# Kernel tuning notes

Hardware: AMD Instinct MI355X
Metric: run time of the kernel (lower is better)

The kernel has to match this reference:

```python
import jax, jax.numpy as jnp
import numpy as np

B, N, C, CD, R = 8, 16384, 32, 256, 32


def setup_inputs() -> dict:
    key = jax.random.key(0)
    ks = jax.random.split(key, 12)
    f32 = jnp.float32
    p = lambda k, shape, s=0.05: jax.random.normal(k, shape, f32) * s
    return {
        "features": jax.random.normal(ks[0], (B, C, N), f32),
        "coords": jax.random.normal(ks[1], (B, 3, N), f32),
        "condition": jax.random.normal(ks[2], (B, CD), f32),
        "conv1_w": p(ks[3], (C, C, 3, 3, 3)), "conv1_b": jnp.zeros((C,), f32),
        "gn1_g": jnp.ones((C,), f32), "gn1_b": jnp.zeros((C,), f32),
        "mod1_w": p(ks[4], (2 * C, CD)),
        "mod1_b": jnp.concatenate([jnp.ones((C,)), jnp.zeros((C,))]).astype(f32),
        "conv2_w": p(ks[5], (C, C, 3, 3, 3)), "conv2_b": jnp.zeros((C,), f32),
        "gn2_g": jnp.ones((C,), f32), "gn2_b": jnp.zeros((C,), f32),
        "mod2_w": p(ks[6], (2 * C, CD)),
        "mod2_b": jnp.concatenate([jnp.ones((C,)), jnp.zeros((C,))]).astype(f32),
        "se_w1": p(ks[7], (C // 8, C)), "se_w2": p(ks[8], (C, C // 8)),
        "pc_w": p(ks[9], (C, C)), "pc_b": jnp.zeros((C,), f32),
        "gnp_g": jnp.ones((C,), f32), "gnp_b": jnp.zeros((C,), f32),
        "modp_w": p(ks[10], (2 * C, CD)),
        "modp_b": jnp.concatenate([jnp.ones((C,)), jnp.zeros((C,))]).astype(f32),
    }


def group_norm(x, g, b, G=8, eps=1e-5):
    shape = x.shape
    xg = x.reshape(shape[0], G, -1)
    m = xg.mean(-1, keepdims=True)
    v = xg.var(-1, keepdims=True)
    xn = ((xg - m) * jax.lax.rsqrt(v + eps)).reshape(shape)
    bshape = (1, shape[1]) + (1,) * (x.ndim - 2)
    return xn * g.reshape(bshape) + b.reshape(bshape)


def adagn(x, c, g, b, mw, mb):
    # GroupNorm then scale/shift from SiLU(c) @ Linear
    x = group_norm(x, g, b)
    m = jax.nn.silu(c) @ mw.T + mb  # (B, 2C)
    scale, shift = jnp.split(m, 2, axis=1)
    bshape = (x.shape[0], x.shape[1]) + (1,) * (x.ndim - 2)
    return x * scale.reshape(bshape) + shift.reshape(bshape)


def voxelize(features, coords, r):
    # scatter-average point features into r^3 grid; coords detached as in torch
    coords = jax.lax.stop_gradient(coords)
    nc = coords - coords.mean(2, keepdims=True)
    denom = jnp.max(jnp.linalg.norm(nc, axis=1, keepdims=True), axis=2, keepdims=True) * 2.0
    nc = nc / denom + 0.5
    nc = jnp.clip(nc * r, 0, r - 1)  # (B,3,N) continuous in [0, r-1]
    vc = jnp.round(nc).astype(jnp.int32)
    idx = (vc[:, 0] * r + vc[:, 1]) * r + vc[:, 2]  # (B,N) flat voxel ids

    def per_batch(f, i):
        s = jax.ops.segment_sum(f.T, i, num_segments=r ** 3)  # (V, D)
        cnt = jax.ops.segment_sum(jnp.ones(i.shape, f.dtype), i, num_segments=r ** 3)
        return (s / jnp.maximum(cnt, 1.0)[:, None]).T.reshape(f.shape[0], r, r, r)

    vox = jax.vmap(per_batch)(features, idx)  # (B, D, r, r, r)
    return vox, nc


def devoxelize(vox, coords, r):
    # trilinear gather of voxel features back to points
    Bv, D = vox.shape[:2]
    flat = vox.reshape(Bv, D, r * r * r)
    lo = jnp.floor(coords)
    frac = coords - lo
    lo = lo.astype(jnp.int32)
    hi = jnp.minimum(lo + 1, r - 1)
    gather = jax.vmap(lambda f, i: f[:, i])  # per-batch (D,V)[:, (N,)] -> (D,N)
    out = jnp.zeros((Bv, D, coords.shape[2]), vox.dtype)
    for dx in (0, 1):
        ix = hi[:, 0] if dx else lo[:, 0]
        wx = frac[:, 0] if dx else 1.0 - frac[:, 0]
        for dy in (0, 1):
            iy = hi[:, 1] if dy else lo[:, 1]
            wy = frac[:, 1] if dy else 1.0 - frac[:, 1]
            for dz in (0, 1):
                iz = hi[:, 2] if dz else lo[:, 2]
                wz = frac[:, 2] if dz else 1.0 - frac[:, 2]
                idx = (ix * r + iy) * r + iz
                out = out + gather(flat, idx) * (wx * wy * wz)[:, None, :]
    return out


def conv3d(x, w, b):
    y = jax.lax.conv_general_dilated(x, w, (1, 1, 1), 'SAME',
                                     dimension_numbers=('NCDHW', 'OIDHW', 'NCDHW'))
    return y + b[None, :, None, None, None]


def reference(features, coords, condition, conv1_w, conv1_b, gn1_g, gn1_b, mod1_w,
              mod1_b, conv2_w, conv2_b, gn2_g, gn2_b, mod2_w, mod2_b, se_w1, se_w2,
              pc_w, pc_b, gnp_g, gnp_b, modp_w, modp_b):
    vox, nc = voxelize(features, coords, R)
    v = conv3d(vox, conv1_w, conv1_b)
    v = jax.nn.silu(adagn(v, condition, gn1_g, gn1_b, mod1_w, mod1_b))
    v = conv3d(v, conv2_w, conv2_b)
    v = adagn(v, condition, gn2_g, gn2_b, mod2_w, mod2_b)
    # SE3d squeeze-excite
    s = jax.nn.sigmoid(jax.nn.relu(v.mean((2, 3, 4)) @ se_w1.T) @ se_w2.T)
    v = v * s[:, :, None, None, None]
    vfeat = devoxelize(v, nc, R)  # (B, C, N)
    # point branch: 1x1 conv + AdaGN + SiLU
    px = jnp.einsum('bdn,od->bon', features, pc_w) + pc_b[None, :, None]
    px = jax.nn.silu(adagn(px, condition, gnp_g, gnp_b, modp_w, modp_b))
    return vfeat + px
```

## Files before the change

kernel.cpp:

```cpp
#include <hip/hip_runtime.h>
#include <math.h>

#define DEV_INLINE __device__ __forceinline__

namespace {

typedef unsigned short u16;
typedef unsigned int u32;
typedef __attribute__((ext_vector_type(8))) short short8v;
typedef __attribute__((ext_vector_type(4))) float f32x4;
typedef __attribute__((ext_vector_type(16))) float f32x16;

constexpr int Bn = 8, Cn = 32, Nn = 16384, Rn = 32, Vn = Rn * Rn * Rn;

DEV_INLINE float siluf(float x) { return x / (1.0f + __expf(-x)); }
DEV_INLINE float bf2f(u16 u) { union { u32 i; float f; } x; x.i = (u32)u << 16; return x.f; }
DEV_INLINE u16 f2bf(float f) {
  union { float f; u32 i; } x; x.f = f;
  return (u16)((x.i + 0x7FFFu + ((x.i >> 16) & 1u)) >> 16);
}
DEV_INLINE u32 pack2(float a, float b) { return (u32)f2bf(a) | ((u32)f2bf(b) << 16); }
DEV_INLINE void unpack8(uint4 u, float* f) {
  f[0] = bf2f(u.x & 0xffff); f[1] = bf2f(u.x >> 16);
  f[2] = bf2f(u.y & 0xffff); f[3] = bf2f(u.y >> 16);
  f[4] = bf2f(u.z & 0xffff); f[5] = bf2f(u.z >> 16);
  f[6] = bf2f(u.w & 0xffff); f[7] = bf2f(u.w >> 16);
}

__global__ void k_cpart1(const float* __restrict__ coords, float* __restrict__ csum) {
  int blk = blockIdx.x;
  int b = blk >> 3, s = blk & 7;
  int t = threadIdx.x;
  const float* cb = coords + (size_t)b * 3 * Nn;
  int n0 = s * 2048;
  float sx = 0.f, sy = 0.f, sz = 0.f;
  for (int n = n0 + t; n < n0 + 2048; n += 256) {
    sx += cb[n]; sy += cb[Nn + n]; sz += cb[2 * Nn + n];
  }
  #pragma unroll
  for (int m = 1; m <= 32; m <<= 1) {
    sx += __shfl_xor(sx, m); sy += __shfl_xor(sy, m); sz += __shfl_xor(sz, m);
  }
  __shared__ float rs[3][4];
  if ((t & 63) == 0) { rs[0][t >> 6] = sx; rs[1][t >> 6] = sy; rs[2][t >> 6] = sz; }
  __syncthreads();
  if (t < 3) atomicAdd(&csum[b * 4 + t], rs[t][0] + rs[t][1] + rs[t][2] + rs[t][3]);
}

__global__ void k_cpart2(const float* __restrict__ coords, const float* __restrict__ csum,
                         int* __restrict__ cmax) {
  int blk = blockIdx.x;
  int b = blk >> 3, s = blk & 7;
  int t = threadIdx.x;
  const float* cb = coords + (size_t)b * 3 * Nn;
  const float invn = 1.0f / (float)Nn;
  float mx = csum[b * 4] * invn, my = csum[b * 4 + 1] * invn, mz = csum[b * 4 + 2] * invn;
  int n0 = s * 2048;
  float mq = 0.f;
  for (int n = n0 + t; n < n0 + 2048; n += 256) {
    float x = cb[n] - mx, y = cb[Nn + n] - my, z = cb[2 * Nn + n] - mz;
    mq = fmaxf(mq, x * x + y * y + z * z);
  }
  #pragma unroll
  for (int m = 1; m <= 32; m <<= 1) mq = fmaxf(mq, __shfl_xor(mq, m));
  __shared__ float rm[4];
  if ((t & 63) == 0) rm[t >> 6] = mq;
  __syncthreads();
  if (t == 0) {
    float v = fmaxf(fmaxf(rm[0], rm[1]), fmaxf(rm[2], rm[3]));
    atomicMax(cmax + b, __float_as_int(v));
  }
}

__global__ void k_cfinal(const float* __restrict__ coords, const float* __restrict__ csum,
                         const int* __restrict__ cmax, float* __restrict__ nc,
                         int* __restrict__ vidx, int* __restrict__ hist) {
  int i = blockIdx.x * 256 + threadIdx.x;
  int b = i >> 14, n = i & (Nn - 1);
  const float* cb = coords + (size_t)b * 3 * Nn;
  const float invn = 1.0f / (float)Nn;
  float mx = csum[b * 4] * invn, my = csum[b * 4 + 1] * invn, mz = csum[b * 4 + 2] * invn;
  float inv = 1.0f / (2.0f * sqrtf(__int_as_float(cmax[b])));
  float x = (cb[n] - mx) * inv + 0.5f;
  float y = (cb[Nn + n] - my) * inv + 0.5f;
  float z = (cb[2 * Nn + n] - mz) * inv + 0.5f;
  x = fminf(fmaxf(x * (float)Rn, 0.f), (float)(Rn - 1));
  y = fminf(fmaxf(y * (float)Rn, 0.f), (float)(Rn - 1));
  z = fminf(fmaxf(z * (float)Rn, 0.f), (float)(Rn - 1));
  float* ncb = nc + (size_t)b * 3 * Nn;
  ncb[n] = x; ncb[Nn + n] = y; ncb[2 * Nn + n] = z;
  int vx = (int)rintf(x), vy = (int)rintf(y), vz = (int)rintf(z);
  int v = (vx * Rn + vy) * Rn + vz;
  vidx[i] = v;
  atomicAdd(&hist[b * Vn + v], 1);
}

__global__ void k_ftr(const float* __restrict__ feat, float* __restrict__ featT) {
  __shared__ float lds[32 * 65];
  int t = threadIdx.x;
  int blk = blockIdx.x;
  int b = blk >> 8, tile = blk & 255;
  int n0 = tile * 64;
  for (int idx = t; idx < 2048; idx += 256) {
    int c = idx >> 6, nn = idx & 63;
    lds[c * 65 + nn] = feat[((size_t)b * 32 + c) * Nn + n0 + nn];
  }
  __syncthreads();
  for (int idx = t; idx < 2048; idx += 256) {
    int n = idx >> 5, c = idx & 31;
    featT[((size_t)b * Nn + n0 + n) * 32 + c] = lds[c * 65 + n];
  }
}

__global__ void k_scan1(const int* __restrict__ hist, int* __restrict__ offs,
                        int* __restrict__ bsum) {
  __shared__ int sd[256];
  int t = threadIdx.x, blk = blockIdx.x;
  int4 h = reinterpret_cast<const int4*>(hist)[blk * 256 + t];
  int s = h.x + h.y + h.z + h.w;
  sd[t] = s; __syncthreads();
  for (int off = 1; off < 256; off <<= 1) {
    int add = (t >= off) ? sd[t - off] : 0;
    __syncthreads();
    sd[t] += add;
    __syncthreads();
  }
  int excl = sd[t] - s;
  int4 o;
  o.x = excl; o.y = excl + h.x; o.z = o.y + h.y; o.w = o.z + h.z;
  reinterpret_cast<int4*>(offs)[blk * 256 + t] = o;
  if (t == 0) bsum[blk] = sd[255];
}

__global__ void k_scan2(const int* __restrict__ bsum, int* __restrict__ bbase) {
  __shared__ int sd[256];
  int t = threadIdx.x;
  int s = bsum[t];
  sd[t] = s; __syncthreads();
  for (int off = 1; off < 256; off <<= 1) {
    int add = (t >= off) ? sd[t - off] : 0;
    __syncthreads();
    sd[t] += add;
    __syncthreads();
  }
  bbase[t] = sd[t] - s;
}

__global__ void k_sortidx(const int* __restrict__ vidx, int* __restrict__ offs,
                          const int* __restrict__ bbase, int* __restrict__ pidx) {
  int i = blockIdx.x * 256 + threadIdx.x;
  int b = i >> 14, n = i & (Nn - 1);
  int g = b * Vn + vidx[i];
  int p = atomicAdd(&offs[g], 1) + bbase[g >> 10];
  pidx[p] = n;
}

__global__ void k_voxavg(const int* __restrict__ hist, const int* __restrict__ offs,
                         const int* __restrict__ bbase, const int* __restrict__ pidx,
                         const float* __restrict__ featT, uint2* __restrict__ vox0) {
  int t = threadIdx.x;
  int wv = blockIdx.x * 4 + (t >> 6);
  int lane = t & 63;
  int c4 = lane & 7, j = lane >> 3;
  int b = wv >> 15;
  int cnt = hist[wv];
  float ax = 0.f, ay = 0.f, az = 0.f, aw = 0.f;
  if (cnt > 0) {
    int end = offs[wv] + bbase[wv >> 10];
    int start = end - cnt;
    const float4* ft = reinterpret_cast<const float4*>(featT) + (size_t)b * Nn * 8;
    for (int k = start + j; k < end; k += 8) {
      int n = pidx[k];
      float4 v = ft[n * 8 + c4];
      ax += v.x; ay += v.y; az += v.z; aw += v.w;
    }
    #pragma unroll
    for (int m = 8; m <= 32; m <<= 1) {
      ax += __shfl_xor(ax, m); ay += __shfl_xor(ay, m);
      az += __shfl_xor(az, m); aw += __shfl_xor(aw, m);
    }
    float invc = 1.0f / (float)cnt;
    ax *= invc; ay *= invc; az *= invc; aw *= invc;
  }
  if (j == 0) {
    uint2 o;
    o.x = pack2(ax, ay);
    o.y = pack2(az, aw);
    vox0[(size_t)wv * 8 + c4] = o;
  }
}

__global__ void k_twz(const float* __restrict__ w, u16* __restrict__ wt) {
  int i = blockIdx.x * 256 + threadIdx.x;
  if (i >= 27 * 32 * 32) return;
  int e = i & 7, l = (i >> 3) & 63, h = (i >> 9) & 1, k = i >> 10;
  int co = l & 31, ci = h * 16 + ((l >> 5) << 3) + e;
  wt[i] = f2bf(w[(co * 32 + ci) * 27 + k]);
}

__global__ void k_mods(const float* __restrict__ cond,
                       const float* __restrict__ w1, const float* __restrict__ b1,
                       const float* __restrict__ w2, const float* __restrict__ b2,
                       const float* __restrict__ wp, const float* __restrict__ bp,
                       float* __restrict__ m1, float* __restrict__ m2,
                       float* __restrict__ mp) {
  int blk = blockIdx.x;
  int mat = blk >> 3, b = blk & 7;
  int t = threadIdx.x;
  __shared__ float sc[256];
  sc[t] = siluf(cond[b * 256 + t]);
  __syncthreads();
  const float* w = (mat == 0) ? w1 : ((mat == 1) ? w2 : wp);
  const float* bb = (mat == 0) ? b1 : ((mat == 1) ? b2 : bp);
  float* dst = (mat == 0) ? m1 : ((mat == 1) ? m2 : mp);
  int wave = t >> 6, lane = t & 63;
  const float4* w4 = reinterpret_cast<const float4*>(w);
  float4 sv = reinterpret_cast<const float4*>(sc)[lane];
  #pragma unroll
  for (int i = 0; i < 16; ++i) {
    int oo = wave * 16 + i;
    float4 wv = w4[oo * 64 + lane];
    float p = wv.x * sv.x + wv.y * sv.y + wv.z * sv.z + wv.w * sv.w;
    #pragma unroll
    for (int m = 1; m <= 32; m <<= 1) p += __shfl_xor(p, m);
    if (lane == 0) dst[b * 64 + oo] = p + bb[oo];
  }
}

__global__ __launch_bounds__(512, 2) void k_conv(
    const u16* __restrict__ in, const u16* __restrict__ wt,
    const float* __restrict__ bias, u16* __restrict__ out) {
  __shared__ uint4 lds_w4[3456];
  __shared__ uint4 lds_x4[4096];
  int t = threadIdx.x;
  int blk = blockIdx.x;
  int yp = blk & 3, x = (blk >> 2) & 31, b = blk >> 7;
  int y0 = yp * 8;
  size_t bbase = (size_t)b * Vn;

  const uint4* gw = reinterpret_cast<const uint4*>(wt);
  for (int i = t; i < 3456; i += 512) lds_w4[i] = gw[i];

  for (int i = t; i < 4080; i += 512) {
    int col = i / 136, rem = i - col * 136;
    int c4 = rem / 34, r = rem - c4 * 34;
    int dxp = col / 10, yy = col - dxp * 10;
    int gx = x + dxp - 1, gy = y0 + yy - 1, z = r - 1;
    uint4 val = make_uint4(0u, 0u, 0u, 0u);
    if (gx >= 0 && gx < 32 && (unsigned)gy < 32u && (unsigned)z < 32u) {
      val = *reinterpret_cast<const uint4*>(
          in + (bbase + (size_t)((gx * 32 + gy) * 32 + z)) * 32 + c4 * 8);
    }
    lds_x4[i] = val;
  }
  __syncthreads();

  int w = t >> 6, lane = t & 63;
  int zc = lane & 31, hi = lane >> 5;
  int y = y0 + w;

  f32x16 acc;
  #pragma unroll
  for (int q = 0; q < 4; ++q) {
    float4 bq = *reinterpret_cast<const float4*>(bias + q * 8 + hi * 4);
    acc[q * 4 + 0] = bq.x; acc[q * 4 + 1] = bq.y;
    acc[q * 4 + 2] = bq.z; acc[q * 4 + 3] = bq.w;
  }

  const u16* lw = reinterpret_cast<const u16*>(lds_w4);
  const u16* lx = reinterpret_cast<const u16*>(lds_x4);

  #pragma unroll
  for (int dxp = 0; dxp < 3; ++dxp) {
    #pragma unroll
    for (int dyp = 0; dyp < 3; ++dyp) {
      int col = dxp * 10 + w + dyp;
      #pragma unroll
      for (int dzp = 0; dzp < 3; ++dzp) {
        int k = (dxp * 3 + dyp) * 3 + dzp;
        short8v a0 = *reinterpret_cast<const short8v*>(lw + ((k * 2 + 0) * 64 + lane) * 8);
        short8v a1 = *reinterpret_cast<const short8v*>(lw + ((k * 2 + 1) * 64 + lane) * 8);
        short8v b0 = *reinterpret_cast<const short8v*>(
            lx + ((col * 4 + hi) * 34 + zc + dzp) * 8);
        short8v b1 = *reinterpret_cast<const short8v*>(
            lx + ((col * 4 + 2 + hi) * 34 + zc + dzp) * 8);
        acc = __builtin_amdgcn_mfma_f32_32x32x16_bf16(a0, b0, acc, 0, 0, 0);
        acc = __builtin_amdgcn_mfma_f32_32x32x16_bf16(a1, b1, acc, 0, 0, 0);
      }
    }
  }

  size_t off = (bbase + (size_t)((x * 32 + y) * 32 + zc)) * 32;
  #pragma unroll
  for (int q = 0; q < 4; ++q) {
    uint2 o;
    o.x = pack2(acc[q * 4 + 0], acc[q * 4 + 1]);
    o.y = pack2(acc[q * 4 + 2], acc[q * 4 + 3]);
    *reinterpret_cast<uint2*>(out + off + q * 8 + hi * 4) = o;
  }
}

__global__ void k_affsilu(uint4* __restrict__ x, const float* __restrict__ Ac,
                          const float* __restrict__ Bc) {
  int i = blockIdx.x * 256 + threadIdx.x;
  int c4 = i & 3, b = i >> 17;
  uint4 v = x[i];
  float f[8];
  unpack8(v, f);
  float4 A0 = reinterpret_cast<const float4*>(Ac)[b * 8 + c4 * 2];
  float4 A1 = reinterpret_cast<const float4*>(Ac)[b * 8 + c4 * 2 + 1];
  float4 B0 = reinterpret_cast<const float4*>(Bc)[b * 8 + c4 * 2];
  float4 B1 = reinterpret_cast<const float4*>(Bc)[b * 8 + c4 * 2 + 1];
  f[0] = siluf(f[0] * A0.x + B0.x); f[1] = siluf(f[1] * A0.y + B0.y);
  f[2] = siluf(f[2] * A0.z + B0.z); f[3] = siluf(f[3] * A0.w + B0.w);
  f[4] = siluf(f[4] * A1.x + B1.x); f[5] = siluf(f[5] * A1.y + B1.y);
  f[6] = siluf(f[6] * A1.z + B1.z); f[7] = siluf(f[7] * A1.w + B1.w);
  uint4 o;
  o.x = pack2(f[0], f[1]); o.y = pack2(f[2], f[3]);
  o.z = pack2(f[4], f[5]); o.w = pack2(f[6], f[7]);
  x[i] = o;
}

__global__ void k_stats_cl(const u16* __restrict__ x, float* __restrict__ psum,
                           float* __restrict__ psq) {
  int blk = blockIdx.x;
  int b = blk >> 5, seg = blk & 31;
  int t = threadIdx.x;
  int c8 = t & 3, vsub = t >> 2;
  float s[8], q[8];
  #pragma unroll
  for (int j = 0; j < 8; ++j) { s[j] = 0.f; q[j] = 0.f; }
  const uint4* xb = reinterpret_cast<const uint4*>(x + (size_t)b * Vn * Cn) +
                    (size_t)seg * 4096;
  for (int it = 0; it < 16; ++it) {
    int v = it * 64 + vsub;
    uint4 u = xb[v * 4 + c8];
    float f[8];
    unpack8(u, f);
    #pragma unroll
    for (int j = 0; j < 8; ++j) { s[j] += f[j]; q[j] += f[j] * f[j]; }
  }
  #pragma unroll
  for (int m = 4; m <= 32; m <<= 1) {
    #pragma unroll
    for (int j = 0; j < 8; ++j) {
      s[j] += __shfl_xor(s[j], m);
      q[j] += __shfl_xor(q[j], m);
    }
  }
  __shared__ float ls[2][4][4][8];
  int wv = t >> 6;
  if ((t & 63) < 4) {
    #pragma unroll
    for (int j = 0; j < 8; ++j) { ls[0][wv][c8][j] = s[j]; ls[1][wv][c8][j] = q[j]; }
  }
  __syncthreads();
  if (t < 64) {
    int arr = t >> 5, c = t & 31;
    float v = ls[arr][0][c >> 3][c & 7] + ls[arr][1][c >> 3][c & 7] +
              ls[arr][2][c >> 3][c & 7] + ls[arr][3][c >> 3][c & 7];
    atomicAdd((arr == 0 ? psum : psq) + b * 32 + c, v);
  }
}

__global__ void k_coef1(const float* __restrict__ psum, const float* __restrict__ psq,
                        const float* __restrict__ mod, const float* __restrict__ g,
                        const float* __restrict__ bgn, float* __restrict__ A,
                        float* __restrict__ Bc) {
  int t = threadIdx.x;
  int b = t >> 5, c = t & 31, grp = c >> 2;
  float s = 0, q = 0;
  for (int j = 0; j < 4; ++j) {
    s += psum[b * 32 + grp * 4 + j];
    q += psq[b * 32 + grp * 4 + j];
  }
  const float cntf = 4.0f * (float)Vn;
  float mean = s / cntf;
  float var = q / cntf - mean * mean;
  float rstd = rsqrtf(var + 1e-5f);
  float scale = mod[b * 64 + c], shift = mod[b * 64 + 32 + c];
  A[t] = rstd * g[c] * scale;
  Bc[t] = (bgn[c] - mean * rstd * g[c]) * scale + shift;
}

__global__ void k_coef2(const float* __restrict__ psum, const float* __restrict__ psq,
                        const float* __restrict__ mod, const float* __restrict__ g,
                        const float* __restrict__ bgn, const float* __restrict__ sw1,
                        const float* __restrict__ sw2, float* __restrict__ S,
                        float* __restrict__ T) {
  __shared__ float zm[8][32];
  __shared__ float hh[8][4];
  int t = threadIdx.x;
  int b = t >> 5, c = t & 31, grp = c >> 2;
  float s = 0, q = 0;
  for (int j = 0; j < 4; ++j) {
    s += psum[b * 32 + grp * 4 + j];
    q += psq[b * 32 + grp * 4 + j];
  }
  const float cntf = 4.0f * (float)Vn;
  float mean = s / cntf;
  float var = q / cntf - mean * mean;
  float rstd = rsqrtf(var + 1e-5f);
  float scale = mod[b * 64 + c], shift = mod[b * 64 + 32 + c];
  float A = rstd * g[c] * scale;
  float Bv = (bgn[c] - mean * rstd * g[c]) * scale + shift;
  float chmean = psum[b * 32 + c] / (float)Vn;
  zm[b][c] = A * chmean + Bv;
  __syncthreads();
  if (t < 32) {
    int b2 = t >> 2, j = t & 3;
    float h = 0;
    for (int cc = 0; cc < 32; ++cc) h += sw1[j * 32 + cc] * zm[b2][cc];
    hh[b2][j] = fmaxf(h, 0.f);
  }
  __syncthreads();
  float sig = 0;
  for (int j = 0; j < 4; ++j) sig += sw2[c * 4 + j] * hh[b][j];
  sig = 1.0f / (1.0f + __expf(-sig));
  S[t] = A * sig;
  T[t] = Bv * sig;
}

__global__ void k_devox(const u16* __restrict__ vox, const float* __restrict__ nc,
                        const float* __restrict__ S, const float* __restrict__ T,
                        float* __restrict__ out) {
  int i = blockIdx.x * 256 + threadIdx.x;
  int b = i >> 14, n = i & (Nn - 1);
  const float* ncb = nc + (size_t)b * 3 * Nn;
  float fx = ncb[n], fy = ncb[Nn + n], fz = ncb[2 * Nn + n];
  float lxf = floorf(fx), lyf = floorf(fy), lzf = floorf(fz);
  float wx1 = fx - lxf, wy1 = fy - lyf, wz1 = fz - lzf;
  int lx = (int)lxf, ly = (int)lyf, lz = (int)lzf;
  int hx = min(lx + 1, 31), hy = min(ly + 1, 31), hz = min(lz + 1, 31);
  float a[32];
  #pragma unroll
  for (int c = 0; c < 32; ++c) a[c] = 0.f;
  for (int corner = 0; corner < 8; ++corner) {
    int cx = (corner & 4) ? hx : lx;
    int cy = (corner & 2) ? hy : ly;
    int cz = (corner & 1) ? hz : lz;
    float ww = ((corner & 4) ? wx1 : 1.f - wx1) *
               ((corner & 2) ? wy1 : 1.f - wy1) *
               ((corner & 1) ? wz1 : 1.f - wz1);
    const uint4* p = reinterpret_cast<const uint4*>(
        vox + ((size_t)b * Vn + (size_t)((cx * 32 + cy) * 32 + cz)) * 32);
    #pragma unroll
    for (int qq = 0; qq < 4; ++qq) {
      float f[8];
      unpack8(p[qq], f);
      #pragma unroll
      for (int j = 0; j < 8; ++j) a[qq * 8 + j] += ww * f[j];
    }
  }
  float* o = out + (size_t)b * 32 * Nn + n;
  #pragma unroll
  for (int c = 0; c < 32; ++c) {
    o[(size_t)c * Nn] = a[c] * S[b * 32 + c] + T[b * 32 + c];
  }
}

__global__ void k_pxlin(const float* __restrict__ feat, const float* __restrict__ w,
                        const float* __restrict__ bias, float* __restrict__ px) {
  __shared__ float lw[1024];
  __shared__ float lb[32];
  int t = threadIdx.x;
  for (int i = t; i < 1024; i += 256) lw[i] = w[i];
  if (t < 32) lb[t] = bias[t];
  __syncthreads();
  int blk = blockIdx.x;
  int b = blk >> 6, tile = blk & 63;
  int n = tile * 256 + t;
  float fr[32];
  const float* fb = feat + (size_t)b * 32 * Nn + n;
  #pragma unroll
  for (int ci = 0; ci < 32; ++ci) fr[ci] = fb[(size_t)ci * Nn];
  float* ob = px + (size_t)b * 32 * Nn + n;
  for (int co = 0; co < 32; ++co) {
    float acc = lb[co];
    #pragma unroll
    for (int ci = 0; ci < 32; ++ci) acc += lw[co * 32 + ci] * fr[ci];
    ob[(size_t)co * Nn] = acc;
  }
}

__global__ void k_statsp(const float* __restrict__ px, float* __restrict__ pgsum,
                         float* __restrict__ pgsq) {
  int blk = blockIdx.x;
  int b = blk >> 5, g = (blk >> 2) & 7, qr = blk & 3;
  const float4* base = reinterpret_cast<const float4*>(
      px + (size_t)b * 32 * Nn + (size_t)g * 4 * Nn) + qr * 4096;
  float s = 0, q = 0;
  int t = threadIdx.x;
  for (int i = t; i < 4096; i += 256) {
    float4 v = base[i];
    s += v.x + v.y + v.z + v.w;
    q += v.x * v.x + v.y * v.y + v.z * v.z + v.w * v.w;
  }
  #pragma unroll
  for (int m = 1; m <= 32; m <<= 1) {
    s += __shfl_xor(s, m);
    q += __shfl_xor(q, m);
  }
  __shared__ float rs[4], rq[4];
  if ((t & 63) == 0) { rs[t >> 6] = s; rq[t >> 6] = q; }
  __syncthreads();
  if (t == 0) {
    atomicAdd(&pgsum[b * 8 + g], rs[0] + rs[1] + rs[2] + rs[3]);
    atomicAdd(&pgsq[b * 8 + g], rq[0] + rq[1] + rq[2] + rq[3]);
  }
}

__global__ void k_coefp(const float* __restrict__ pgsum, const float* __restrict__ pgsq,
                        const float* __restrict__ mod, const float* __restrict__ g,
                        const float* __restrict__ bgn, float* __restrict__ A,
                        float* __restrict__ Bc) {
  int t = threadIdx.x;
  int b = t >> 5, c = t & 31, grp = c >> 2;
  float m = pgsum[b * 8 + grp] / 65536.f;
  float var = pgsq[b * 8 + grp] / 65536.f - m * m;
  float r = rsqrtf(var + 1e-5f);
  float scale = mod[b * 64 + c], shift = mod[b * 64 + 32 + c];
  A[t] = r * g[c] * scale;
  Bc[t] = (bgn[c] - m * r * g[c]) * scale + shift;
}

__global__ void k_final(const float* __restrict__ px, const float* __restrict__ A,
                        const float* __restrict__ Bc, float* __restrict__ out) {
  int i = blockIdx.x * 256 + threadIdx.x;
  int bc = i >> 14;
  float y = px[i] * A[bc] + Bc[bc];
  out[i] += siluf(y);
}

}

extern "C" void kernel_launch(void* const* d_in, const int* in_sizes, int n_in,
                              void* d_out, int out_size, void* d_ws, size_t ws_size,
                              hipStream_t stream) {
  (void)in_sizes; (void)n_in; (void)out_size; (void)ws_size;
  const float* features = (const float*)d_in[0];
  const float* coords = (const float*)d_in[1];
  const float* condition = (const float*)d_in[2];
  const float* conv1_w = (const float*)d_in[3];
  const float* conv1_b = (const float*)d_in[4];
  const float* gn1_g = (const float*)d_in[5];
  const float* gn1_b = (const float*)d_in[6];
  const float* mod1_w = (const float*)d_in[7];
  const float* mod1_b = (const float*)d_in[8];
  const float* conv2_w = (const float*)d_in[9];
  const float* conv2_b = (const float*)d_in[10];
  const float* gn2_g = (const float*)d_in[11];
  const float* gn2_b = (const float*)d_in[12];
  const float* mod2_w = (const float*)d_in[13];
  const float* mod2_b = (const float*)d_in[14];
  const float* se_w1 = (const float*)d_in[15];
  const float* se_w2 = (const float*)d_in[16];
  const float* pc_w = (const float*)d_in[17];
  const float* pc_b = (const float*)d_in[18];
  const float* gnp_g = (const float*)d_in[19];
  const float* gnp_b = (const float*)d_in[20];
  const float* modp_w = (const float*)d_in[21];
  const float* modp_b = (const float*)d_in[22];

  char* w = (char*)d_ws;
  float* featT = (float*)w;
  u16* vox1 = (u16*)w;
  float* px = (float*)w;
  u16* vox2 = (u16*)(w + 16777216);
  w += 33554432;
  u16* vox0 = (u16*)w; w += 16777216;
  int* hist = (int*)w;  w += 1048576;
  float* psum1 = (float*)w; w += 1024;
  float* psq1 = (float*)w;  w += 1024;
  float* psum2 = (float*)w; w += 1024;
  float* psq2 = (float*)w;  w += 1024;
  float* pgsum = (float*)w; w += 256;
  float* pgsq = (float*)w;  w += 256;
  float* csum = (float*)w;  w += 128;
  int* cmax = (int*)w;      w += 64;
  int* offs = (int*)w;  w += 1048576;
  int* bsum = (int*)w;  w += 1024;
  int* bbase = (int*)w; w += 1024;
  int* pidx = (int*)w;  w += 524288;
  float* ncb = (float*)w;   w += 1572864;
  int* vidx = (int*)w;      w += 524288;
  u16* wt1b = (u16*)w;      w += 55296;
  u16* wt2b = (u16*)w;      w += 55296;
  float* m1 = (float*)w;    w += 2048;
  float* m2 = (float*)w;    w += 2048;
  float* mp = (float*)w;    w += 2048;
  float* A1 = (float*)w;    w += 1024;
  float* B1 = (float*)w;    w += 1024;
  float* Sc = (float*)w;    w += 1024;
  float* Tc = (float*)w;    w += 1024;
  float* Ap = (float*)w;    w += 1024;
  float* Bp = (float*)w;    w += 1024;
  float* out = (float*)d_out;

  hipMemsetAsync(hist, 0, 1048576 + 4096 + 512 + 192, stream);

  k_cpart1<<<Bn * 8, 256, 0, stream>>>(coords, csum);
  k_ftr<<<Bn * 256, 256, 0, stream>>>(features, featT);
  k_twz<<<108, 256, 0, stream>>>(conv1_w, wt1b);
  k_twz<<<108, 256, 0, stream>>>(conv2_w, wt2b);
  k_mods<<<24, 256, 0, stream>>>(condition, mod1_w, mod1_b, mod2_w, mod2_b,
                                 modp_w, modp_b, m1, m2, mp);
  k_cpart2<<<Bn * 8, 256, 0, stream>>>(coords, csum, cmax);
  k_cfinal<<<(Bn * Nn) / 256, 256, 0, stream>>>(coords, csum, cmax, ncb, vidx, hist);
  k_scan1<<<256, 256, 0, stream>>>(hist, offs, bsum);
  k_scan2<<<1, 256, 0, stream>>>(bsum, bbase);
  k_sortidx<<<(Bn * Nn) / 256, 256, 0, stream>>>(vidx, offs, bbase, pidx);
  k_voxavg<<<(Bn * Vn) / 4, 256, 0, stream>>>(hist, offs, bbase, pidx, featT,
                                              (uint2*)vox0);
  k_conv<<<1024, 512, 0, stream>>>(vox0, wt1b, conv1_b, vox1);
  k_stats_cl<<<256, 256, 0, stream>>>(vox1, psum1, psq1);
  k_coef1<<<1, 256, 0, stream>>>(psum1, psq1, m1, gn1_g, gn1_b, A1, B1);
  k_affsilu<<<4096, 256, 0, stream>>>((uint4*)vox1, A1, B1);
  k_conv<<<1024, 512, 0, stream>>>(vox1, wt2b, conv2_b, vox2);
  k_stats_cl<<<256, 256, 0, stream>>>(vox2, psum2, psq2);
  k_coef2<<<1, 256, 0, stream>>>(psum2, psq2, m2, gn2_g, gn2_b, se_w1, se_w2, Sc, Tc);
  k_devox<<<(Bn * Nn) / 256, 256, 0, stream>>>(vox2, ncb, Sc, Tc, out);
  k_pxlin<<<Bn * 64, 256, 0, stream>>>(features, pc_w, pc_b, px);
  k_statsp<<<256, 256, 0, stream>>>(px, pgsum, pgsq);
  k_coefp<<<1, 256, 0, stream>>>(pgsum, pgsq, mp, gnp_g, gnp_b, Ap, Bp);
  k_final<<<(Bn * Cn * Nn) / 256, 256, 0, stream>>>(px, Ap, Bp, out);
}
```

Before: 234.9 us.

## Fuse GroupNorm stats into conv epilogue and point branch into devox

The conv kernel now reduces per-channel sums and squares of its accumulators in the epilogue and writes per-block partials. This removes the two separate stats passes over the voxel grid. The point-branch linear layer is merged with the feature transpose and stores its output as bf16 channel-last. A small stats kernel reads that output, and the devoxelize kernel applies the point AdaGN+SiLU and adds it, which replaces the separate stats, final and read-modify-write passes over the output. In exchange the point-branch intermediate is held in bf16, and the conv epilogue gets extra shuffles and LDS reductions.

```diff
diff --git a/kernel.cpp b/kernel.cpp
--- a/kernel.cpp
+++ b/kernel.cpp
@@ -8,7 +8,6 @@
 typedef unsigned short u16;
 typedef unsigned int u32;
 typedef __attribute__((ext_vector_type(8))) short short8v;
-typedef __attribute__((ext_vector_type(4))) float f32x4;
 typedef __attribute__((ext_vector_type(16))) float f32x16;
 
 constexpr int Bn = 8, Cn = 32, Nn = 16384, Rn = 32, Vn = Rn * Rn * Rn;
@@ -95,20 +94,52 @@
   atomicAdd(&hist[b * Vn + v], 1);
 }
 
-__global__ void k_ftr(const float* __restrict__ feat, float* __restrict__ featT) {
-  __shared__ float lds[32 * 65];
-  int t = threadIdx.x;
+__global__ __launch_bounds__(256, 2) void k_pxlin(
+    const float* __restrict__ feat, const float* __restrict__ w,
+    const float* __restrict__ bias, float* __restrict__ featT,
+    u16* __restrict__ pxb) {
+  __shared__ float lw[1024];
+  __shared__ float lb[32];
+  __shared__ float lbuf[256 * 33];
+  int t = threadIdx.x;
+  for (int i = t; i < 1024; i += 256) lw[i] = w[i];
+  if (t < 32) lb[t] = bias[t];
   int blk = blockIdx.x;
-  int b = blk >> 8, tile = blk & 255;
-  int n0 = tile * 64;
-  for (int idx = t; idx < 2048; idx += 256) {
-    int c = idx >> 6, nn = idx & 63;
-    lds[c * 65 + nn] = feat[((size_t)b * 32 + c) * Nn + n0 + nn];
-  }
-  __syncthreads();
-  for (int idx = t; idx < 2048; idx += 256) {
-    int n = idx >> 5, c = idx & 31;
-    featT[((size_t)b * Nn + n0 + n) * 32 + c] = lds[c * 65 + n];
+  int b = blk >> 6, tile = blk & 63;
+  int n0 = tile * 256, n = n0 + t;
+  float fr[32];
+  const float* fb = feat + (size_t)b * 32 * Nn + n;
+  #pragma unroll
+  for (int ci = 0; ci < 32; ++ci) {
+    fr[ci] = fb[(size_t)ci * Nn];
+    lbuf[t * 33 + ci] = fr[ci];
+  }
+  __syncthreads();
+  float* ftb = featT + ((size_t)b * Nn + n0) * 32;
+  #pragma unroll
+  for (int j = 0; j < 32; ++j) {
+    int idx = j * 256 + t;
+    ftb[idx] = lbuf[(idx >> 5) * 33 + (idx & 31)];
+  }
+  __syncthreads();
+  u32* lbu = reinterpret_cast<u32*>(lbuf);
+  #pragma unroll
+  for (int p2 = 0; p2 < 16; ++p2) {
+    int co0 = p2 * 2;
+    float a0 = lb[co0], a1 = lb[co0 + 1];
+    #pragma unroll
+    for (int ci = 0; ci < 32; ++ci) {
+      a0 += lw[co0 * 32 + ci] * fr[ci];
+      a1 += lw[(co0 + 1) * 32 + ci] * fr[ci];
+    }
+    lbu[t * 17 + p2] = pack2(a0, a1);
+  }
+  __syncthreads();
+  u32* pxu = reinterpret_cast<u32*>(pxb) + ((size_t)b * Nn + n0) * 16;
+  #pragma unroll
+  for (int j = 0; j < 16; ++j) {
+    int idx = j * 256 + t;
+    pxu[idx] = lbu[(idx >> 4) * 17 + (idx & 15)];
   }
 }
 
@@ -229,7 +260,8 @@
 
 __global__ __launch_bounds__(512, 2) void k_conv(
     const u16* __restrict__ in, const u16* __restrict__ wt,
-    const float* __restrict__ bias, u16* __restrict__ out) {
+    const float* __restrict__ bias, u16* __restrict__ out,
+    float* __restrict__ pstat) {
   __shared__ uint4 lds_w4[3456];
   __shared__ uint4 lds_x4[4096];
   int t = threadIdx.x;
@@ -297,6 +329,36 @@
     o.x = pack2(acc[q * 4 + 0], acc[q * 4 + 1]);
     o.y = pack2(acc[q * 4 + 2], acc[q * 4 + 3]);
     *reinterpret_cast<uint2*>(out + off + q * 8 + hi * 4) = o;
+  }
+
+  float s16[16], q16[16];
+  #pragma unroll
+  for (int r = 0; r < 16; ++r) { s16[r] = acc[r]; q16[r] = acc[r] * acc[r]; }
+  #pragma unroll
+  for (int m = 1; m <= 16; m <<= 1) {
+    #pragma unroll
+    for (int r = 0; r < 16; ++r) {
+      s16[r] += __shfl_xor(s16[r], m);
+      q16[r] += __shfl_xor(q16[r], m);
+    }
+  }
+  __syncthreads();
+  float* sred = reinterpret_cast<float*>(lds_w4);
+  if ((lane & 31) == 0) {
+    #pragma unroll
+    for (int r = 0; r < 16; ++r) {
+      int co = (r & 3) + 8 * (r >> 2) + 4 * hi;
+      sred[w * 64 + co] = s16[r];
+      sred[512 + w * 64 + co] = q16[r];
+    }
+  }
+  __syncthreads();
+  if (t < 64) {
+    int arr = t >> 5, c = t & 31;
+    const float* bp_ = sred + arr * 512 + c;
+    float v = bp_[0] + bp_[64] + bp_[128] + bp_[192] +
+              bp_[256] + bp_[320] + bp_[384] + bp_[448];
+    pstat[blk * 64 + arr * 32 + c] = v;
   }
 }
 
@@ -321,17 +383,16 @@
   x[i] = o;
 }
 
-__global__ void k_stats_cl(const u16* __restrict__ x, float* __restrict__ psum,
-                           float* __restrict__ psq) {
+__global__ void k_statspx(const u16* __restrict__ x, float* __restrict__ psum,
+                          float* __restrict__ psq, int segs) {
   int blk = blockIdx.x;
-  int b = blk >> 5, seg = blk & 31;
+  int b = blk / segs;
   int t = threadIdx.x;
   int c8 = t & 3, vsub = t >> 2;
   float s[8], q[8];
   #pragma unroll
   for (int j = 0; j < 8; ++j) { s[j] = 0.f; q[j] = 0.f; }
-  const uint4* xb = reinterpret_cast<const uint4*>(x + (size_t)b * Vn * Cn) +
-                    (size_t)seg * 4096;
+  const uint4* xb = reinterpret_cast<const uint4*>(x) + (size_t)blk * 4096;
   for (int it = 0; it < 16; ++it) {
     int v = it * 64 + vsub;
     uint4 u = xb[v * 4 + c8];
@@ -363,48 +424,60 @@
   }
 }
 
-__global__ void k_coef1(const float* __restrict__ psum, const float* __restrict__ psq,
-                        const float* __restrict__ mod, const float* __restrict__ g,
-                        const float* __restrict__ bgn, float* __restrict__ A,
-                        float* __restrict__ Bc) {
-  int t = threadIdx.x;
-  int b = t >> 5, c = t & 31, grp = c >> 2;
-  float s = 0, q = 0;
-  for (int j = 0; j < 4; ++j) {
-    s += psum[b * 32 + grp * 4 + j];
-    q += psq[b * 32 + grp * 4 + j];
-  }
+__global__ void k_coef1(const float* __restrict__ pstat, const float* __restrict__ mod,
+                        const float* __restrict__ g, const float* __restrict__ bgn,
+                        float* __restrict__ A, float* __restrict__ Bc) {
+  int t = threadIdx.x;
+  int b = t >> 5, c = t & 31;
+  float cs = 0.f, cq = 0.f;
+  const float* p = pstat + (size_t)b * 128 * 64;
+  for (int i = 0; i < 128; ++i) {
+    cs += p[i * 64 + c];
+    cq += p[i * 64 + 32 + c];
+  }
+  __shared__ float ls[256], lq[256];
+  ls[t] = cs; lq[t] = cq;
+  __syncthreads();
+  int gb = t & ~3;
+  float s4 = ls[gb] + ls[gb + 1] + ls[gb + 2] + ls[gb + 3];
+  float q4 = lq[gb] + lq[gb + 1] + lq[gb + 2] + lq[gb + 3];
   const float cntf = 4.0f * (float)Vn;
-  float mean = s / cntf;
-  float var = q / cntf - mean * mean;
+  float mean = s4 / cntf;
+  float var = q4 / cntf - mean * mean;
   float rstd = rsqrtf(var + 1e-5f);
   float scale = mod[b * 64 + c], shift = mod[b * 64 + 32 + c];
   A[t] = rstd * g[c] * scale;
   Bc[t] = (bgn[c] - mean * rstd * g[c]) * scale + shift;
 }
 
-__global__ void k_coef2(const float* __restrict__ psum, const float* __restrict__ psq,
-                        const float* __restrict__ mod, const float* __restrict__ g,
-                        const float* __restrict__ bgn, const float* __restrict__ sw1,
-                        const float* __restrict__ sw2, float* __restrict__ S,
-                        float* __restrict__ T) {
+__global__ void k_coef2(const float* __restrict__ pstat, const float* __restrict__ mod,
+                        const float* __restrict__ g, const float* __restrict__ bgn,
+                        const float* __restrict__ sw1, const float* __restrict__ sw2,
+                        float* __restrict__ S, float* __restrict__ T) {
   __shared__ float zm[8][32];
   __shared__ float hh[8][4];
-  int t = threadIdx.x;
-  int b = t >> 5, c = t & 31, grp = c >> 2;
-  float s = 0, q = 0;
-  for (int j = 0; j < 4; ++j) {
-    s += psum[b * 32 + grp * 4 + j];
-    q += psq[b * 32 + grp * 4 + j];
-  }
+  __shared__ float ls[256], lq[256];
+  int t = threadIdx.x;
+  int b = t >> 5, c = t & 31;
+  float cs = 0.f, cq = 0.f;
+  const float* p = pstat + (size_t)b * 128 * 64;
+  for (int i = 0; i < 128; ++i) {
+    cs += p[i * 64 + c];
+    cq += p[i * 64 + 32 + c];
+  }
+  ls[t] = cs; lq[t] = cq;
+  __syncthreads();
+  int gb = t & ~3;
+  float s4 = ls[gb] + ls[gb + 1] + ls[gb + 2] + ls[gb + 3];
+  float q4 = lq[gb] + lq[gb + 1] + lq[gb + 2] + lq[gb + 3];
   const float cntf = 4.0f * (float)Vn;
-  float mean = s / cntf;
-  float var = q / cntf - mean * mean;
+  float mean = s4 / cntf;
+  float var = q4 / cntf - mean * mean;
   float rstd = rsqrtf(var + 1e-5f);
   float scale = mod[b * 64 + c], shift = mod[b * 64 + 32 + c];
   float A = rstd * g[c] * scale;
   float Bv = (bgn[c] - mean * rstd * g[c]) * scale + shift;
-  float chmean = psum[b * 32 + c] / (float)Vn;
+  float chmean = cs / (float)Vn;
   zm[b][c] = A * chmean + Bv;
   __syncthreads();
   if (t < 32) {
@@ -421,9 +494,31 @@
   T[t] = Bv * sig;
 }
 
-__global__ void k_devox(const u16* __restrict__ vox, const float* __restrict__ nc,
-                        const float* __restrict__ S, const float* __restrict__ T,
-                        float* __restrict__ out) {
+__global__ void k_coefp(const float* __restrict__ psum, const float* __restrict__ psq,
+                        const float* __restrict__ mod, const float* __restrict__ g,
+                        const float* __restrict__ bgn, float* __restrict__ A,
+                        float* __restrict__ Bc) {
+  __shared__ float ls[256], lq[256];
+  int t = threadIdx.x;
+  int b = t >> 5, c = t & 31;
+  ls[t] = psum[t]; lq[t] = psq[t];
+  __syncthreads();
+  int gb = t & ~3;
+  float s4 = ls[gb] + ls[gb + 1] + ls[gb + 2] + ls[gb + 3];
+  float q4 = lq[gb] + lq[gb + 1] + lq[gb + 2] + lq[gb + 3];
+  const float cntf = 4.0f * (float)Nn;
+  float m = s4 / cntf;
+  float var = q4 / cntf - m * m;
+  float r = rsqrtf(var + 1e-5f);
+  float scale = mod[b * 64 + c], shift = mod[b * 64 + 32 + c];
+  A[t] = r * g[c] * scale;
+  Bc[t] = (bgn[c] - m * r * g[c]) * scale + shift;
+}
+
+__global__ void k_devoxfinal(const u16* __restrict__ vox, const float* __restrict__ nc,
+                             const u16* __restrict__ pxb, const float* __restrict__ S,
+                             const float* __restrict__ T, const float* __restrict__ Ap,
+                             const float* __restrict__ Bp, float* __restrict__ out) {
   int i = blockIdx.x * 256 + threadIdx.x;
   int b = i >> 14, n = i & (Nn - 1);
   const float* ncb = nc + (size_t)b * 3 * Nn;
@@ -452,84 +547,19 @@
       for (int j = 0; j < 8; ++j) a[qq * 8 + j] += ww * f[j];
     }
   }
+  const uint4* pp = reinterpret_cast<const uint4*>(pxb) + (size_t)i * 4;
   float* o = out + (size_t)b * 32 * Nn + n;
   #pragma unroll
-  for (int c = 0; c < 32; ++c) {
-    o[(size_t)c * Nn] = a[c] * S[b * 32 + c] + T[b * 32 + c];
-  }
-}
-
-__global__ void k_pxlin(const float* __restrict__ feat, const float* __restrict__ w,
-                        const float* __restrict__ bias, float* __restrict__ px) {
-  __shared__ float lw[1024];
-  __shared__ float lb[32];
-  int t = threadIdx.x;
-  for (int i = t; i < 1024; i += 256) lw[i] = w[i];
-  if (t < 32) lb[t] = bias[t];
-  __syncthreads();
-  int blk = blockIdx.x;
-  int b = blk >> 6, tile = blk & 63;
-  int n = tile * 256 + t;
-  float fr[32];
-  const float* fb = feat + (size_t)b * 32 * Nn + n;
-  #pragma unroll
-  for (int ci = 0; ci < 32; ++ci) fr[ci] = fb[(size_t)ci * Nn];
-  float* ob = px + (size_t)b * 32 * Nn + n;
-  for (int co = 0; co < 32; ++co) {
-    float acc = lb[co];
-    #pragma unroll
-    for (int ci = 0; ci < 32; ++ci) acc += lw[co * 32 + ci] * fr[ci];
-    ob[(size_t)co * Nn] = acc;
-  }
-}
-
-__global__ void k_statsp(const float* __restrict__ px, float* __restrict__ pgsum,
-                         float* __restrict__ pgsq) {
-  int blk = blockIdx.x;
-  int b = blk >> 5, g = (blk >> 2) & 7, qr = blk & 3;
-  const float4* base = reinterpret_cast<const float4*>(
-      px + (size_t)b * 32 * Nn + (size_t)g * 4 * Nn) + qr * 4096;
-  float s = 0, q = 0;
-  int t = threadIdx.x;
-  for (int i = t; i < 4096; i += 256) {
-    float4 v = base[i];
-    s += v.x + v.y + v.z + v.w;
-    q += v.x * v.x + v.y * v.y + v.z * v.z + v.w * v.w;
-  }
-  #pragma unroll
-  for (int m = 1; m <= 32; m <<= 1) {
-    s += __shfl_xor(s, m);
-    q += __shfl_xor(q, m);
-  }
-  __shared__ float rs[4], rq[4];
-  if ((t & 63) == 0) { rs[t >> 6] = s; rq[t >> 6] = q; }
-  __syncthreads();
-  if (t == 0) {
-    atomicAdd(&pgsum[b * 8 + g], rs[0] + rs[1] + rs[2] + rs[3]);
-    atomicAdd(&pgsq[b * 8 + g], rq[0] + rq[1] + rq[2] + rq[3]);
-  }
-}
-
-__global__ void k_coefp(const float* __restrict__ pgsum, const float* __restrict__ pgsq,
-                        const float* __restrict__ mod, const float* __restrict__ g,
-                        const float* __restrict__ bgn, float* __restrict__ A,
-                        float* __restrict__ Bc) {
-  int t = threadIdx.x;
-  int b = t >> 5, c = t & 31, grp = c >> 2;
-  float m = pgsum[b * 8 + grp] / 65536.f;
-  float var = pgsq[b * 8 + grp] / 65536.f - m * m;
-  float r = rsqrtf(var + 1e-5f);
-  float scale = mod[b * 64 + c], shift = mod[b * 64 + 32 + c];
-  A[t] = r * g[c] * scale;
-  Bc[t] = (bgn[c] - m * r * g[c]) * scale + shift;
-}
-
-__global__ void k_final(const float* __restrict__ px, const float* __restrict__ A,
-                        const float* __restrict__ Bc, float* __restrict__ out) {
-  int i = blockIdx.x * 256 + threadIdx.x;
-  int bc = i >> 14;
-  float y = px[i] * A[bc] + Bc[bc];
-  out[i] += siluf(y);
+  for (int qq = 0; qq < 4; ++qq) {
+    float pf[8];
+    unpack8(pp[qq], pf);
+    #pragma unroll
+    for (int j = 0; j < 8; ++j) {
+      int c = qq * 8 + j;
+      float y = pf[j] * Ap[b * 32 + c] + Bp[b * 32 + c];
+      o[(size_t)c * Nn] = a[c] * S[b * 32 + c] + T[b * 32 + c] + siluf(y);
+    }
+  }
 }
 
 }
@@ -565,17 +595,13 @@
   char* w = (char*)d_ws;
   float* featT = (float*)w;
   u16* vox1 = (u16*)w;
-  float* px = (float*)w;
-  u16* vox2 = (u16*)(w + 16777216);
-  w += 33554432;
+  w += 16777216;
+  u16* vox2 = (u16*)w; w += 16777216;
   u16* vox0 = (u16*)w; w += 16777216;
+  u16* pxb = (u16*)w;  w += 8388608;
   int* hist = (int*)w;  w += 1048576;
-  float* psum1 = (float*)w; w += 1024;
-  float* psq1 = (float*)w;  w += 1024;
-  float* psum2 = (float*)w; w += 1024;
-  float* psq2 = (float*)w;  w += 1024;
-  float* pgsum = (float*)w; w += 256;
-  float* pgsq = (float*)w;  w += 256;
+  float* psump = (float*)w; w += 1024;
+  float* psqp = (float*)w;  w += 1024;
   float* csum = (float*)w;  w += 128;
   int* cmax = (int*)w;      w += 64;
   int* offs = (int*)w;  w += 1048576;
@@ -586,6 +612,8 @@
   int* vidx = (int*)w;      w += 524288;
   u16* wt1b = (u16*)w;      w += 55296;
   u16* wt2b = (u16*)w;      w += 55296;
+  float* pstat1 = (float*)w; w += 262144;
+  float* pstat2 = (float*)w; w += 262144;
   float* m1 = (float*)w;    w += 2048;
   float* m2 = (float*)w;    w += 2048;
   float* mp = (float*)w;    w += 2048;
@@ -597,14 +625,16 @@
   float* Bp = (float*)w;    w += 1024;
   float* out = (float*)d_out;
 
-  hipMemsetAsync(hist, 0, 1048576 + 4096 + 512 + 192, stream);
-
+  hipMemsetAsync(hist, 0, 1048576 + 1024 + 1024 + 128 + 64, stream);
+
+  k_pxlin<<<Bn * 64, 256, 0, stream>>>(features, pc_w, pc_b, featT, pxb);
   k_cpart1<<<Bn * 8, 256, 0, stream>>>(coords, csum);
-  k_ftr<<<Bn * 256, 256, 0, stream>>>(features, featT);
   k_twz<<<108, 256, 0, stream>>>(conv1_w, wt1b);
   k_twz<<<108, 256, 0, stream>>>(conv2_w, wt2b);
   k_mods<<<24, 256, 0, stream>>>(condition, mod1_w, mod1_b, mod2_w, mod2_b,
                                  modp_w, modp_b, m1, m2, mp);
+  k_statspx<<<Bn * 16, 256, 0, stream>>>(pxb, psump, psqp, 16);
+  k_coefp<<<1, 256, 0, stream>>>(psump, psqp, mp, gnp_g, gnp_b, Ap, Bp);
   k_cpart2<<<Bn * 8, 256, 0, stream>>>(coords, csum, cmax);
   k_cfinal<<<(Bn * Nn) / 256, 256, 0, stream>>>(coords, csum, cmax, ncb, vidx, hist);
   k_scan1<<<256, 256, 0, stream>>>(hist, offs, bsum);
@@ -612,16 +642,10 @@
   k_sortidx<<<(Bn * Nn) / 256, 256, 0, stream>>>(vidx, offs, bbase, pidx);
   k_voxavg<<<(Bn * Vn) / 4, 256, 0, stream>>>(hist, offs, bbase, pidx, featT,
                                               (uint2*)vox0);
-  k_conv<<<1024, 512, 0, stream>>>(vox0, wt1b, conv1_b, vox1);
-  k_stats_cl<<<256, 256, 0, stream>>>(vox1, psum1, psq1);
-  k_coef1<<<1, 256, 0, stream>>>(psum1, psq1, m1, gn1_g, gn1_b, A1, B1);
+  k_conv<<<1024, 512, 0, stream>>>(vox0, wt1b, conv1_b, vox1, pstat1);
+  k_coef1<<<1, 256, 0, stream>>>(pstat1, m1, gn1_g, gn1_b, A1, B1);
   k_affsilu<<<4096, 256, 0, stream>>>((uint4*)vox1, A1, B1);
-  k_conv<<<1024, 512, 0, stream>>>(vox1, wt2b, conv2_b, vox2);
-  k_stats_cl<<<256, 256, 0, stream>>>(vox2, psum2, psq2);
-  k_coef2<<<1, 256, 0, stream>>>(psum2, psq2, m2, gn2_g, gn2_b, se_w1, se_w2, Sc, Tc);
-  k_devox<<<(Bn * Nn) / 256, 256, 0, stream>>>(vox2, ncb, Sc, Tc, out);
-  k_pxlin<<<Bn * 64, 256, 0, stream>>>(features, pc_w, pc_b, px);
-  k_statsp<<<256, 256, 0, stream>>>(px, pgsum, pgsq);
-  k_coefp<<<1, 256, 0, stream>>>(pgsum, pgsq, mp, gnp_g, gnp_b, Ap, Bp);
-  k_final<<<(Bn * Cn * Nn) / 256, 256, 0, stream>>>(px, Ap, Bp, out);
-}
+  k_conv<<<1024, 512, 0, stream>>>(vox1, wt2b, conv2_b, vox2, pstat2);
+  k_coef2<<<1, 256, 0, stream>>>(pstat2, m2, gn2_g, gn2_b, se_w1, se_w2, Sc, Tc);
+  k_devoxfinal<<<(Bn * Nn) / 256, 256, 0, stream>>>(vox2, ncb, pxb, Sc, Tc, Ap, Bp, out);
+}
```

After: 240.7 us. 1.02x slower.
